# Kernel optimization log

Measured on AMD Instinct MI355X. Metric: run time of the kernel, lower is better.

## Reference

```python
import jax, jax.numpy as jnp
from jax import lax
import numpy as np

B, T, F_IN = 256, 128, 16
H, L, OUT = 512, 3, 16  # hidden_size, rnn_depth, dim_state*2


def setup_inputs() -> dict:
    key = jax.random.key(0)
    ks = jax.random.split(key, 5)
    scale_in = 1.0 / np.sqrt(F_IN)
    scale_h = 1.0 / np.sqrt(2 * H)
    return {
        "x": jax.random.normal(ks[0], (B, T, F_IN), jnp.float32),
        "proj_w": jax.random.normal(ks[1], (F_IN, H), jnp.float32) * scale_in,
        "proj_b": jnp.zeros((H,), jnp.float32),
        "lstm_w": jax.random.normal(ks[2], (L, 2 * H, 4 * H), jnp.float32) * scale_h,
        "lstm_b": jnp.zeros((L, 4 * H), jnp.float32),
        "out_w": jax.random.normal(ks[3], (H, OUT), jnp.float32) * (1.0 / np.sqrt(H)),
        "out_b": jnp.zeros((OUT,), jnp.float32),
    }


def reference(x, proj_w, proj_b, lstm_w, lstm_b, out_w, out_b):
    # x: [B, T, F_in]
    b, t, _ = x.shape
    n_layers, _, h4 = lstm_w.shape
    h = h4 // 4

    # Projection + relu -> all LSTM layers see H-dim inputs
    xp = jax.nn.relu(jnp.einsum("btf,fh->bth", x, proj_w) + proj_b)  # [B,T,H]

    def step(carry, xt):
        hs_prev, cs_prev = carry  # each [L, B, H]
        inp = xt  # [B, H]
        hs, cs = [], []
        for l in range(n_layers):
            gated = jnp.concatenate([inp, hs_prev[l]], axis=-1) @ lstm_w[l] + lstm_b[l]
            i, g, f, o = jnp.split(gated, 4, axis=-1)
            c_new = jax.nn.sigmoid(f + 1.0) * cs_prev[l] + jax.nn.sigmoid(i) * jnp.tanh(g)
            h_new = jax.nn.sigmoid(o) * jnp.tanh(c_new)
            hs.append(h_new)
            cs.append(c_new)
            # relu between layers (rnn_activation), not after the last layer
            inp = jax.nn.relu(h_new) if l < n_layers - 1 else h_new
        return (jnp.stack(hs), jnp.stack(cs)), inp

    zeros = jnp.zeros((n_layers, b, h), xp.dtype)
    xs = jnp.swapaxes(xp, 0, 1)  # [T, B, H] for scan over time
    _, ys = lax.scan(step, (zeros, zeros), xs)
    y = jnp.swapaxes(ys, 0, 1)  # [B, T, H]
    return jnp.einsum("bth,ho->bto", y, out_w) + out_b
```

## Files before the change

kernel.cpp:

```cpp
#include <hip/hip_runtime.h>


typedef __attribute__((ext_vector_type(8)))  short bf16x8;
typedef __attribute__((ext_vector_type(16))) float f32x16;
typedef __attribute__((ext_vector_type(8)))  unsigned short us8;

#define B_  256
#define T_  128
#define FIN 16
#define H_  512
#define G4  2048
#define SLAB 131072
#define MF(A,B,C) __builtin_amdgcn_mfma_f32_32x32x16_bf16(A,B,C,0,0,0)

static __device__ __forceinline__ float bf2f(unsigned short u){
  return __uint_as_float(((unsigned)u) << 16);
}
static __device__ __forceinline__ unsigned short f2bf(float f){
  unsigned u = __float_as_uint(f);
  u += 0x7fffu + ((u >> 16) & 1u);
  return (unsigned short)(u >> 16);
}
static __device__ __forceinline__ float sigm(float x){ return 1.f/(1.f + __expf(-x)); }
static __device__ __forceinline__ float tanh_(float x){ return 1.f - 2.f/(__expf(2.f*x) + 1.f); }

static __device__ __forceinline__ void wave_wait(const int* slotbase, int v){
  int guard = 0;
  for (;;){
    int s = __hip_atomic_load((const int*)(slotbase + (threadIdx.x & 31)),
                              __ATOMIC_RELAXED, __HIP_MEMORY_SCOPE_AGENT);
    if (__all(s >= v) || guard++ > (1 << 17)) break;
    __builtin_amdgcn_s_sleep(2);
  }
  asm volatile("" ::: "memory");
}


__global__ __launch_bounds__(256) void k_wconv(const float* __restrict__ w,
                                               unsigned short* __restrict__ wfo){
  long idx = (long)blockIdx.x*256 + threadIdx.x;
  int lane = (int)(idx & 63);
  int s    = (int)((idx >> 6) & 63);
  int Jb   = (int)((idx >> 12) & 63);
  int l    = (int)(idx >> 18);
  int jp = Jb*32 + (lane & 31);
  int co = (jp & 3)*512 + (jp >> 2);
  int k0 = s*16 + (lane >> 5)*8;
  us8 o;
  #pragma unroll
  for (int e = 0; e < 8; ++e)
    o[e] = f2bf(w[((long)(l*1024 + k0 + e))*2048 + co]);
  *(us8*)(wfo + idx*8) = o;
}

__global__ __launch_bounds__(256) void k_xp(const float* __restrict__ x,
                                            const float* __restrict__ pw,
                                            const float* __restrict__ pb,
                                            unsigned short* __restrict__ xpt){
  __shared__ float sw[FIN*H_];
  __shared__ float sb[H_];
  int tid = threadIdx.x;
  for (int i = tid; i < FIN*H_; i += 256) sw[i] = pw[i];
  for (int i = tid; i < H_;     i += 256) sb[i] = pb[i];
  __syncthreads();
  int r0 = blockIdx.x * 64;
  int c0 = tid * 2;
  int s  = c0 >> 4, kl = c0 & 15;
  for (int rr = 0; rr < 64; ++rr){
    int r = r0 + rr;
    int b = r >> 7, t = r & 127;
    const float* xr = x + (long)r*FIN;
    float a0 = sb[c0], a1 = sb[c0+1];
    #pragma unroll
    for (int f = 0; f < FIN; ++f){
      float xv = xr[f];
      a0 += xv * sw[f*H_ + c0];
      a1 += xv * sw[f*H_ + c0 + 1];
    }
    ushort2 tmp;
    tmp.x = f2bf(fmaxf(a0, 0.f));
    tmp.y = f2bf(fmaxf(a1, 0.f));
    long off = (long)t*SLAB
             + ((((b>>7)*4 + ((b>>5)&3))*32 + s) << 9)
             + ((b&31) + ((kl>>3)<<5))*8 + (kl&7);
    *(ushort2*)(xpt + off) = tmp;
  }
}

__global__ __launch_bounds__(256) void k_out(const unsigned short* __restrict__ ring,
                                             const float* __restrict__ ow,
                                             const float* __restrict__ ob,
                                             float* __restrict__ dout){
  __shared__ float sw[H_*16];
  int tid = threadIdx.x;
  for (int i = tid; i < H_*16; i += 256) sw[i] = ow[i];
  __syncthreads();
  int r0 = blockIdx.x * 16;
  int rr = tid >> 4, o = tid & 15;
  int r = r0 + rr;
  int b = r >> 7, t = r & 127;
  long tb = ((long)t*3 + 2)*SLAB + (((b>>7)*4 + ((b>>5)&3)) << 14);
  float acc = ob[o];
  for (int k8 = 0; k8 < 64; ++k8){
    long off = tb + ((long)(k8 >> 1) << 9) + ((b&31) + ((k8&1)<<5))*8;
    us8 v = *(const us8*)(ring + off);
    #pragma unroll
    for (int e = 0; e < 8; ++e) acc += bf2f(v[e]) * sw[(k8*8 + e)*16 + o];
  }
  dout[(long)r*16 + o] = acc;
}


#define DMA1(I) { \
  __builtin_amdgcn_global_load_lds( \
    (const __attribute__((address_space(1))) void*)(gsrc + (I)*512), \
    (__attribute__((address_space(3))) void*)(actb + (((I) & 7) << 10)), 16, 0, 0); }

#define ISSUE4(G) { DMA1((G)*4+0) DMA1((G)*4+1) DMA1((G)*4+2) DMA1((G)*4+3) }

#define WVM(N) { asm volatile("s_waitcnt vmcnt(" #N ")" ::: "memory"); \
                 __builtin_amdgcn_sched_barrier(0); }
#define LGK0   { asm volatile("s_waitcnt lgkmcnt(0)" ::: "memory"); \
                 __builtin_amdgcn_sched_barrier(0); }

#define CONS(I, RELU) { \
  bf16x8 w0 = *(const bf16x8*)(Wl + (((SB + (I))*64 + lane) << 4)); \
  bf16x8 w1 = *(const bf16x8*)(Wl + (65536 + (((SB + (I))*64 + lane) << 4))); \
  bf16x8 b  = *(const bf16x8*)(actb + (((I) & 7) << 10) + (lane << 4)); \
  if (RELU){ _Pragma("unroll") for (int e = 0; e < 8; ++e) if (b[e] < 0) b[e] = 0; } \
  a0 = MF(w0, b, a0); a1 = MF(w1, b, a1); }

#define CONS4(G, R) { CONS((G)*4+0,R) CONS((G)*4+1,R) CONS((G)*4+2,R) CONS((G)*4+3,R) }

#define GEMM_HALF(R) { \
  ISSUE4(0) ISSUE4(1) \
  WVM(4) CONS4(0,R) LGK0 ISSUE4(2) \
  WVM(4) CONS4(1,R) LGK0 ISSUE4(3) \
  WVM(4) CONS4(2,R) LGK0 ISSUE4(4) \
  WVM(4) CONS4(3,R) LGK0 ISSUE4(5) \
  WVM(4) CONS4(4,R) LGK0 ISSUE4(6) \
  WVM(4) CONS4(5,R) LGK0 ISSUE4(7) \
  WVM(4) CONS4(6,R) \
  WVM(0) CONS4(7,R) }

#define CELL1(A, JB) { _Pragma("unroll") \
  for (int q = 0; q < 4; ++q){ \
    float iv = A[4*q+0], gv = A[4*q+1], fv = A[4*q+2], ov = A[4*q+3]; \
    float cp = cs##JB[q]; \
    float cn = sigm(fv + 1.f)*cp + sigm(iv)*tanh_(gv); \
    float hn = sigm(ov)*tanh_(cn); \
    cs##JB[q] = cn; \
    hst[l31*24 + JB*8 + 2*q + l5] = f2bf(hn); } }

__global__ __launch_bounds__(256, 1) void k_rnn(
    const unsigned short* __restrict__ wf, const float* __restrict__ lb,
    unsigned short* ownring, unsigned short* crossring,
    const unsigned short* __restrict__ xpt,
    int* stepslots, int* xcdslots, int sepAvail)
{
  extern __shared__ unsigned char Wl[];
  const int bid = blockIdx.x;
  const int g = bid & 7;
  if (g >= 6) return;
  const int l = g >> 1, mg = g & 1;
  const int n = bid >> 3;
  const int tid = threadIdx.x;
  const int lane = tid & 63;
  const int wv = tid >> 6;
  const int l5 = lane >> 5, l31 = lane & 31;
  const int tilebase = (mg*4 + wv) << 5;
  unsigned char* actb = Wl + 131072 + (wv << 13);
  unsigned short* hst = (unsigned short*)actb;

  {
    const us8* src = (const us8*)(wf + ((long)(l*64 + n*2))*4096*8);
    us8* dst = (us8*)Wl;
    for (int i = tid; i < 8192; i += 256) dst[i] = src[i];
  }
  f32x16 bias0, bias1;
  #pragma unroll
  for (int r = 0; r < 16; ++r){
    int hc0 = (n*2 + 0)*8 + 2*(r>>2) + l5;
    int hc1 = (n*2 + 1)*8 + 2*(r>>2) + l5;
    bias0[r] = lb[l*G4 + (r&3)*512 + hc0];
    bias1[r] = lb[l*G4 + (r&3)*512 + hc1];
  }
  float cs0[4] = {0.f,0.f,0.f,0.f}, cs1[4] = {0.f,0.f,0.f,0.f};
  __syncthreads();

  unsigned myxcd = 0;
  asm volatile("s_getreg_b32 %0, hwreg(HW_REG_XCC_ID)" : "=s"(myxcd));
  if (tid == 0)
    __hip_atomic_store(xcdslots + g*32 + n, 1 + (int)myxcd,
                       __ATOMIC_RELAXED, __HIP_MEMORY_SCOPE_AGENT);
  int uni;
  {
    int guard = 0, s = 0;
    for (;;){
      s = __hip_atomic_load((const int*)(xcdslots + g*32 + (lane & 31)),
                            __ATOMIC_RELAXED, __HIP_MEMORY_SCOPE_AGENT);
      if (__all(s >= 1) || guard++ > (1 << 17)) break;
      __builtin_amdgcn_s_sleep(2);
    }
    uni = __all(s == 1 + (int)myxcd);
    asm volatile("" ::: "memory");
  }
  const int ownSep = (sepAvail && uni) ? 1 : 0;
  const unsigned short* ownr = ownSep ? ownring : crossring;

  const int* sOwn  = stepslots + g*32;
  const int* sPrev = stepslots + (g - 2)*32;
  int* mySlot = stepslots + g*32 + n;

  for (int t = 0; t < T_; ++t){
    f32x16 a0 = bias0, a1 = bias1;

    if (l == 0){
      {
        const unsigned short* gsrc = xpt + (long)t*SLAB + ((long)tilebase << 9)
                                   + lane*8;
        const int SB = 0;
        GEMM_HALF(0)
      }
      if (t > 0){
        wave_wait(sOwn, t);
        const unsigned short* gsrc = ownr + ((long)(t-1)*3 + l)*SLAB
                                   + ((long)tilebase << 9) + lane*8;
        const int SB = 32;
        GEMM_HALF(0)
      }
    } else {
      if (t > 0){
        wave_wait(sOwn, t);
        const unsigned short* gsrc = ownr + ((long)(t-1)*3 + l)*SLAB
                                   + ((long)tilebase << 9) + lane*8;
        const int SB = 32;
        GEMM_HALF(0)
      }
      wave_wait(sPrev, t + 1);
      {
        const unsigned short* gsrc = crossring + ((long)t*3 + (l-1))*SLAB
                                   + ((long)tilebase << 9) + lane*8;
        const int SB = 0;
        GEMM_HALF(1)
      }
    }

    CELL1(a0, 0)
    CELL1(a1, 1)
    asm volatile("s_waitcnt lgkmcnt(0)" ::: "memory");
    __builtin_amdgcn_sched_barrier(0);
    {
      us8 v = *(const us8*)(hst + l31*24 + l5*8);
      long off = ((long)t*3 + l)*SLAB + ((long)(tilebase + n) << 9) + lane*8;
      if (ownSep) *(us8*)(ownring + off) = v;
      *(volatile us8*)(crossring + off) = v;
    }
    __syncthreads();
    if (tid == 0)
      __hip_atomic_store(mySlot, t + 1, __ATOMIC_RELAXED, __HIP_MEMORY_SCOPE_AGENT);
  }
}


__global__ __launch_bounds__(256) void k_wconv0(const float* __restrict__ w,
                                                unsigned short* __restrict__ wf){
  long d8 = ((long)blockIdx.x*256 + threadIdx.x) * 8;
  int lane = (int)((d8 >> 3) & 63);
  int s    = (int)((d8 >> 9) & 31);
  int J    = (int)((d8 >> 14) & 127);
  int l    = (int)(d8 >> 21);
  int jj = lane & 15, khi = lane >> 4;
  int jp = J*16 + jj;
  int co = (jp & 3)*512 + (jp >> 2);
  int kbase = s*32 + khi*8;
  us8 o;
  #pragma unroll
  for (int e = 0; e < 8; ++e)
    o[e] = f2bf(w[((long)(l*1024 + kbase + e))*2048 + co]);
  *(us8*)(wf + d8) = o;
}

__global__ void k_iout(float* __restrict__ dout, const float* __restrict__ ob){
  int i = blockIdx.x*256 + threadIdx.x;
  if (i < B_*T_*16) dout[i] = ob[i & 15];
}

__global__ __launch_bounds__(256, 2) void k_stage0(
    const float* __restrict__ x, const float* __restrict__ pw, const float* __restrict__ pb,
    const unsigned short* __restrict__ wf, const float* __restrict__ lb,
    const float* __restrict__ ow, float* __restrict__ dout,
    float* __restrict__ cbuf, unsigned short* __restrict__ hb,
    int t, int l)
{
  __shared__ unsigned char Ab[32*2048];
  __shared__ float gsm[32*36];
  __shared__ float xrow[32*16];
  __shared__ float hcell[32*8];

  const int tid = threadIdx.x;
  const int bid = blockIdx.x;
  const int m = bid >> 6;
  const int n = ((bid & 7) << 3) | ((bid >> 3) & 7);
  const int pwr = t & 1, prd = pwr ^ 1;
  const int bg0 = m * 32;

  {
    const unsigned short* src = hb + (((long)prd*3 + l)*256 + bg0)*512;
    for (int i = 0; i < 8; ++i){
      int cid = tid + 256*i;
      int row = cid >> 6, cc = cid & 63;
      us8 v = *(const us8*)(src + (long)row*512 + cc*8);
      *(us8*)(Ab + ((row*2048 + 1024 + cc*16) ^ ((row & 7) << 4))) = v;
    }
  }
  if (l > 0){
    const unsigned short* src = hb + (((long)pwr*3 + (l-1))*256 + bg0)*512;
    for (int i = 0; i < 8; ++i){
      int cid = tid + 256*i;
      int row = cid >> 6, cc = cid & 63;
      us8 v = *(const us8*)(src + (long)row*512 + cc*8);
      #pragma unroll
      for (int e = 0; e < 8; ++e) v[e] = (v[e] & 0x8000u) ? (unsigned short)0 : v[e];
      *(us8*)(Ab + ((row*2048 + cc*16) ^ ((row & 7) << 4))) = v;
    }
  } else {
    {
      int e2 = tid*2;
      int br = e2 >> 4, f = e2 & 15;
      const float* xr = x + ((long)(bg0 + br)*T_ + t)*FIN;
      xrow[e2] = xr[f]; xrow[e2+1] = xr[f+1];
    }
    __syncthreads();
    for (int i = 0; i < 8; ++i){
      int cid = tid + 256*i;
      int row = cid >> 6, cc = cid & 63;
      int c0 = cc*8;
      us8 vv;
      #pragma unroll
      for (int j = 0; j < 8; ++j){
        float a = pb[c0 + j];
        #pragma unroll
        for (int f = 0; f < FIN; ++f) a += xrow[row*16 + f] * pw[f*H_ + c0 + j];
        vv[j] = f2bf(fmaxf(a, 0.f));
      }
      *(us8*)(Ab + ((row*2048 + cc*16) ^ ((row & 7) << 4))) = vv;
    }
  }
  __syncthreads();

  const int lane = tid & 63, wid = tid >> 6;
  const int wm = wid >> 1, wn = wid & 1;
  const int J = n*2 + wn;
  const int arow = wm*16 + (lane & 15);
  const unsigned abase = (unsigned)arow*2048 + ((lane >> 4) << 4);
  const unsigned axor = (unsigned)((arow & 7) << 4);
  const unsigned short* bp = wf + ((((long)l*128 + J)*32)*64 + lane)*8;

  typedef __attribute__((ext_vector_type(4))) float f32x4;
  f32x4 acc = {0.f, 0.f, 0.f, 0.f};
  #pragma unroll
  for (int s = 0; s < 32; ++s){
    bf16x8 af = *(const bf16x8*)(Ab + ((abase + s*64) ^ axor));
    bf16x8 bfr = *(const bf16x8*)(bp + (long)s*512);
    acc = __builtin_amdgcn_mfma_f32_16x16x32_bf16(af, bfr, acc, 0, 0, 0);
  }
  {
    int colb = wn*16 + (lane & 15);
    int rowb = wm*16 + ((lane >> 4) << 2);
    #pragma unroll
    for (int r = 0; r < 4; ++r) gsm[(rowb + r)*36 + colb] = acc[r];
  }
  __syncthreads();

  {
    int bl = tid >> 3, hc = tid & 7;
    float4 g4 = *(float4*)(&gsm[bl*36 + hc*4]);
    int hcol = n*8 + hc;
    int bgl = bg0 + bl;
    float iv = g4.x + lb[l*G4 + hcol];
    float gv = g4.y + lb[l*G4 + 512 + hcol];
    float fv = g4.z + lb[l*G4 + 1024 + hcol];
    float ov = g4.w + lb[l*G4 + 1536 + hcol];
    long coff = ((long)l*256 + bgl)*512 + hcol;
    float cp = cbuf[coff];
    float cn = sigm(fv + 1.f)*cp + sigm(iv)*tanh_(gv);
    float hn = sigm(ov)*tanh_(cn);
    cbuf[coff] = cn;
    hb[(((long)pwr*3 + l)*256 + bgl)*512 + hcol] = f2bf(hn);
    if (l == 2) hcell[bl*8 + hc] = hn;
  }
  if (l == 2){
    __syncthreads();
    #pragma unroll
    for (int q = 0; q < 2; ++q){
      int oid = tid + 256*q;
      int bl = oid >> 4, o = oid & 15;
      float a = 0.f;
      #pragma unroll
      for (int hc = 0; hc < 8; ++hc) a += hcell[bl*8 + hc] * ow[(n*8 + hc)*16 + o];
      atomicAdd(dout + ((long)(bg0 + bl)*T_ + t)*16 + o, a);
    }
  }
}


extern "C" void kernel_launch(void* const* d_in, const int* in_sizes, int n_in,
                              void* d_out, int out_size, void* d_ws, size_t ws_size,
                              hipStream_t stream)
{
  const float* x  = (const float*)d_in[0];
  const float* pw = (const float*)d_in[1];
  const float* pb = (const float*)d_in[2];
  const float* lw = (const float*)d_in[3];
  const float* lb = (const float*)d_in[4];
  const float* ow = (const float*)d_in[5];
  const float* ob = (const float*)d_in[6];
  float* dout = (float*)d_out;

  const size_t RING = 128ull*3*SLAB*2;
  char* ws = (char*)d_ws;
  size_t off = 0;
  auto carve = [&](size_t bytes){ char* p = ws + off; off += (bytes + 255) & ~(size_t)255; return p; };

  unsigned short* wf    = (unsigned short*)carve(3ull*64*4096*8*2);
  unsigned short* cross = (unsigned short*)carve(RING);
  unsigned short* xpt   = (unsigned short*)carve(128ull*SLAB*2);
  int*            steps = (int*)carve(1024);
  int*            xcds  = (int*)carve(1024);
  size_t need_mid = off;
  unsigned short* own   = (unsigned short*)carve(RING);
  size_t need_lux = off;

  int mode = (ws_size >= need_lux) ? 2 : (ws_size >= need_mid ? 1 : 0);
  if (mode){
    if (hipFuncSetAttribute((const void*)k_rnn,
                            hipFuncAttributeMaxDynamicSharedMemorySize,
                            163840) != hipSuccess)
      mode = 0;
  }

  if (mode){
    int sepAvail = (mode == 2) ? 1 : 0;
    unsigned short* ownp = sepAvail ? own : cross;
    hipMemsetAsync(steps, 0, 2048, stream);
    k_wconv<<<3072, 256, 0, stream>>>(lw, wf);
    k_xp<<<512, 256, 0, stream>>>(x, pw, pb, xpt);
    k_rnn<<<256, 256, 163840, stream>>>(wf, lb, ownp, cross, xpt,
                                        steps, xcds, sepAvail);
    k_out<<<2048, 256, 0, stream>>>(cross, ow, ob, dout);
  } else {
    size_t o2 = 0;
    auto carve2 = [&](size_t bytes){ char* p = ws + o2; o2 += (bytes + 255) & ~(size_t)255; return p; };
    unsigned short* wf0   = (unsigned short*)carve2(3ull*1024*2048*2);
    float*          cbuf0 = (float*)carve2(3ull*256*512*4);
    unsigned short* hbuf0 = (unsigned short*)carve2(2ull*3*256*512*2);
    hipMemsetAsync(cbuf0, 0, 3ull*256*512*4 + 2ull*3*256*512*2, stream);
    k_wconv0<<<3072, 256, 0, stream>>>(lw, wf0);
    k_iout<<<2048, 256, 0, stream>>>(dout, ob);
    for (int t = 0; t < T_; ++t)
      for (int l = 0; l < 3; ++l)
        k_stage0<<<512, 256, 0, stream>>>(x, pw, pb, wf0, lb, ow, dout,
                                          cbuf0, hbuf0, t, l);
  }
}
```

Measured before the change: 1.335 ms.

## Hold recurrent-half LSTM weights in registers and run the input half first

Each wave now loads the recurrent (hidden-state) half of its LSTM weight slice into registers once, in 64 bf16x8 values, before the time loop. That half's MFMAs read weights from registers, not LDS, which removes LDS weight traffic from the step that sits on the recurrence critical path. The step order also changes for every layer: the input or lower-layer half is computed first and the own-layer recurrent half last, so the wait on the same layer's previous step is pushed later. The cost is a large rise in register pressure that could cause spills, and deeper layers now wait on the lower layer before doing any work.

```diff
diff --git a/kernel.cpp b/kernel.cpp
--- a/kernel.cpp
+++ b/kernel.cpp
@@ -124,15 +124,20 @@
                  __builtin_amdgcn_sched_barrier(0); }
 
 #define CONS(I, RELU) { \
-  bf16x8 w0 = *(const bf16x8*)(Wl + (((SB + (I))*64 + lane) << 4)); \
-  bf16x8 w1 = *(const bf16x8*)(Wl + (65536 + (((SB + (I))*64 + lane) << 4))); \
+  bf16x8 w0 = *(const bf16x8*)(Wl + (((I)*64 + lane) << 4)); \
+  bf16x8 w1 = *(const bf16x8*)(Wl + (65536 + (((I)*64 + lane) << 4))); \
   bf16x8 b  = *(const bf16x8*)(actb + (((I) & 7) << 10) + (lane << 4)); \
   if (RELU){ _Pragma("unroll") for (int e = 0; e < 8; ++e) if (b[e] < 0) b[e] = 0; } \
   a0 = MF(w0, b, a0); a1 = MF(w1, b, a1); }
 
-#define CONS4(G, R) { CONS((G)*4+0,R) CONS((G)*4+1,R) CONS((G)*4+2,R) CONS((G)*4+3,R) }
-
-#define GEMM_HALF(R) { \
+#define CONSR(I) { \
+  bf16x8 b = *(const bf16x8*)(actb + (((I) & 7) << 10) + (lane << 4)); \
+  a0 = MF(wr0[I], b, a0); a1 = MF(wr1[I], b, a1); }
+
+#define CONS4(G, R)  { CONS((G)*4+0,R) CONS((G)*4+1,R) CONS((G)*4+2,R) CONS((G)*4+3,R) }
+#define CONSR4(G)    { CONSR((G)*4+0) CONSR((G)*4+1) CONSR((G)*4+2) CONSR((G)*4+3) }
+
+#define GEMM_HALF_L(R) { \
   ISSUE4(0) ISSUE4(1) \
   WVM(4) CONS4(0,R) LGK0 ISSUE4(2) \
   WVM(4) CONS4(1,R) LGK0 ISSUE4(3) \
@@ -142,6 +147,17 @@
   WVM(4) CONS4(5,R) LGK0 ISSUE4(7) \
   WVM(4) CONS4(6,R) \
   WVM(0) CONS4(7,R) }
+
+#define GEMM_HALF_R { \
+  ISSUE4(0) ISSUE4(1) \
+  WVM(4) CONSR4(0) LGK0 ISSUE4(2) \
+  WVM(4) CONSR4(1) LGK0 ISSUE4(3) \
+  WVM(4) CONSR4(2) LGK0 ISSUE4(4) \
+  WVM(4) CONSR4(3) LGK0 ISSUE4(5) \
+  WVM(4) CONSR4(4) LGK0 ISSUE4(6) \
+  WVM(4) CONSR4(5) LGK0 ISSUE4(7) \
+  WVM(4) CONSR4(6) \
+  WVM(0) CONSR4(7) }
 
 #define CELL1(A, JB) { _Pragma("unroll") \
   for (int q = 0; q < 4; ++q){ \
@@ -172,10 +188,18 @@
   unsigned char* actb = Wl + 131072 + (wv << 13);
   unsigned short* hst = (unsigned short*)actb;
 
+  const unsigned short* wbase = wf + ((long)(l*64 + n*2))*4096*8;
+
   {
-    const us8* src = (const us8*)(wf + ((long)(l*64 + n*2))*4096*8);
+    const us8* src = (const us8*)wbase;
     us8* dst = (us8*)Wl;
     for (int i = tid; i < 8192; i += 256) dst[i] = src[i];
+  }
+  bf16x8 wr0[32], wr1[32];
+  #pragma unroll
+  for (int i = 0; i < 32; ++i){
+    wr0[i] = *(const bf16x8*)(wbase + ((long)((32+i)*64 + lane))*8);
+    wr1[i] = *(const bf16x8*)(wbase + 32768 + ((long)((32+i)*64 + lane))*8);
   }
   f32x16 bias0, bias1;
   #pragma unroll
@@ -210,40 +234,26 @@
 
   const int* sOwn  = stepslots + g*32;
   const int* sPrev = stepslots + (g - 2)*32;
-  int* mySlot = stepslots + g*32 + n;
+  int* myFlag = stepslots + g*32 + n;
 
   for (int t = 0; t < T_; ++t){
     f32x16 a0 = bias0, a1 = bias1;
 
     if (l == 0){
-      {
-        const unsigned short* gsrc = xpt + (long)t*SLAB + ((long)tilebase << 9)
-                                   + lane*8;
-        const int SB = 0;
-        GEMM_HALF(0)
-      }
-      if (t > 0){
-        wave_wait(sOwn, t);
-        const unsigned short* gsrc = ownr + ((long)(t-1)*3 + l)*SLAB
-                                   + ((long)tilebase << 9) + lane*8;
-        const int SB = 32;
-        GEMM_HALF(0)
-      }
+      const unsigned short* gsrc = xpt + (long)t*SLAB + ((long)tilebase << 9)
+                                 + lane*8;
+      GEMM_HALF_L(0)
     } else {
-      if (t > 0){
-        wave_wait(sOwn, t);
-        const unsigned short* gsrc = ownr + ((long)(t-1)*3 + l)*SLAB
-                                   + ((long)tilebase << 9) + lane*8;
-        const int SB = 32;
-        GEMM_HALF(0)
-      }
       wave_wait(sPrev, t + 1);
-      {
-        const unsigned short* gsrc = crossring + ((long)t*3 + (l-1))*SLAB
-                                   + ((long)tilebase << 9) + lane*8;
-        const int SB = 0;
-        GEMM_HALF(1)
-      }
+      const unsigned short* gsrc = crossring + ((long)t*3 + (l-1))*SLAB
+                                 + ((long)tilebase << 9) + lane*8;
+      GEMM_HALF_L(1)
+    }
+    if (t > 0){
+      wave_wait(sOwn, t);
+      const unsigned short* gsrc = ownr + ((long)(t-1)*3 + l)*SLAB
+                                 + ((long)tilebase << 9) + lane*8;
+      GEMM_HALF_R
     }
 
     CELL1(a0, 0)
@@ -258,7 +268,7 @@
     }
     __syncthreads();
     if (tid == 0)
-      __hip_atomic_store(mySlot, t + 1, __ATOMIC_RELAXED, __HIP_MEMORY_SCOPE_AGENT);
+      __hip_atomic_store(myFlag, t + 1, __ATOMIC_RELAXED, __HIP_MEMORY_SCOPE_AGENT);
   }
 }
 
```

Result: faster. 1.225 ms (-8.2%).
